# Kernel optimization log

Hardware: AMD Instinct MI355X
Metric: run time of the kernel (lower is better)

## Reference

```python
import jax, jax.numpy as jnp
import numpy as np

NUM_ITEMS, NUM_USERS, H = 100000, 16384, 48
GCN, ATTN, HID, TOW = 128, 128, 256, 256


def setup_inputs() -> dict:
    key = jax.random.key(0)
    ks = jax.random.split(key, 20)
    s = 0.02
    return {
        'item_feat': jax.random.normal(ks[0], (NUM_ITEMS, 2), jnp.float32),
        'gcn_item_emb': jax.random.normal(ks[1], (NUM_ITEMS, GCN), jnp.float32),
        'gcn_user_emb': jax.random.normal(ks[2], (NUM_USERS, GCN), jnp.float32),
        'hist_idx': jax.random.randint(ks[3], (NUM_USERS, H), 0, NUM_ITEMS, jnp.int32),
        'hist_len': jax.random.randint(ks[4], (NUM_USERS,), 0, H, jnp.int32),
        'Wi1': s * jax.random.normal(ks[5], (GCN + 2, HID), jnp.float32),
        'bi1': jnp.zeros((HID,), jnp.float32),
        'Wi2': s * jax.random.normal(ks[6], (HID, TOW), jnp.float32),
        'bi2': jnp.zeros((TOW,), jnp.float32),
        'Wq': s * jax.random.normal(ks[7], (GCN, ATTN), jnp.float32),
        'bq': jnp.zeros((ATTN,), jnp.float32),
        'Wk': s * jax.random.normal(ks[8], (TOW, ATTN), jnp.float32),
        'bk': jnp.zeros((ATTN,), jnp.float32),
        'Wu1': s * jax.random.normal(ks[9], (GCN + TOW, HID), jnp.float32),
        'bu1': jnp.zeros((HID,), jnp.float32),
        'Wu2': s * jax.random.normal(ks[10], (HID, TOW), jnp.float32),
        'bu2': jnp.zeros((TOW,), jnp.float32),
    }


def _l2norm(x):
    # F.normalize(dim=1): divide by L2 norm clamped to 1e-12
    n = jnp.sqrt(jnp.sum(x * x, axis=1, keepdims=True))
    return x / jnp.maximum(n, 1e-12)


def reference(item_feat, gcn_item_emb, gcn_user_emb, hist_idx, hist_len,
              Wi1, bi1, Wi2, bi2, Wq, bq, Wk, bk, Wu1, bu1, Wu2, bu2):
    # encode_items: [N, 130] -> MLP -> normalized [N, TOW]
    xi = jnp.concatenate([item_feat, gcn_item_emb], axis=1)
    h = jax.nn.relu(xi @ Wi1 + bi1)
    item_emb = _l2norm(h @ Wi2 + bi2)

    # encode_users (batched ragged attention with padding mask)
    item_vecs = item_emb[hist_idx]                       # [U, H, TOW]
    q = gcn_user_emb @ Wq + bq                           # [U, ATTN]
    k = item_vecs @ Wk + bk                              # [U, H, ATTN]
    scores = jnp.einsum('ud,uhd->uh', q, k) / jnp.sqrt(jnp.float32(ATTN))
    mask = jnp.arange(H)[None, :] <= hist_len[:, None]   # >= 1 valid per user
    attn = jax.nn.softmax(jnp.where(mask, scores, -1e30), axis=1)
    hist = jnp.einsum('uh,uhd->ud', attn, item_vecs)     # [U, TOW]
    fused = jnp.concatenate([gcn_user_emb, hist], axis=1)  # [U, 384]
    hu = jax.nn.relu(fused @ Wu1 + bu1)
    user_emb = _l2norm(hu @ Wu2 + bu2)
    return user_emb
```

## Files before the change

### kernel.cpp

```cpp
#include <hip/hip_runtime.h>
#include <hip/hip_bf16.h>
#include <hip/hip_fp8.h>
#include <math.h>

#define NITEMS 100000
#define NUSERS 16384
#define HLEN   48
#define GCN    128
#define ATTN_D 128
#define HID    256
#define TOW    256

typedef __attribute__((ext_vector_type(8))) short short8;
typedef __attribute__((ext_vector_type(16))) unsigned char uchar16;
typedef __attribute__((ext_vector_type(4))) float f32x4;
typedef __hip_bfloat16 bf16;

static __device__ __forceinline__ float bfu(unsigned short u) {
  unsigned int x = ((unsigned int)u) << 16;
  float f; __builtin_memcpy(&f, &x, 4); return f;
}
static __device__ __forceinline__ short f2bf(float v) {
  bf16 h = __float2bfloat16(v);
  short s; __builtin_memcpy(&s, &h, 2); return s;
}
static __device__ __forceinline__ unsigned char f2e4m3(float v) {
  __hip_fp8_e4m3 t(v);
  return (unsigned char)t.__x;
}
static __device__ __forceinline__ float e4m3f(unsigned char b) {
  __hip_fp8_e4m3 t;
  t.__x = (__hip_fp8_storage_t)b;
  return (float)t;
}

#define GLDS16(g, l)                                                            \
  __builtin_amdgcn_global_load_lds(                                             \
      (const __attribute__((address_space(1))) unsigned int*)(g),               \
      (__attribute__((address_space(3))) unsigned int*)(l), 16, 0, 0)

__global__ __launch_bounds__(256) void k_prep_w(const float* __restrict__ W,
                                                bf16* __restrict__ out,
                                                int Korig, int KS, int NT, int perm) {
  int tid = blockIdx.x * 256 + threadIdx.x;
  int total = KS * NT * 512;
  if (tid >= total) return;
  int i  = tid & 7;
  int l  = (tid >> 3) & 63;
  int ct = (tid >> 9) % NT;
  int ks = (tid >> 9) / NT;
  int k   = ks * 32 + ((l >> 4) << 3) + i;
  int col = ct * 16 + (l & 15);
  int N = NT * 16;
  int srck = perm ? ((k < 128) ? (k + 2) : (k - 128)) : k;
  float v = (k < Korig) ? W[(size_t)srck * N + col] : 0.f;
  out[tid] = __float2bfloat16(v);
}

__global__ __launch_bounds__(256) void k_prep_w8(const float* __restrict__ W,
                                                 unsigned char* __restrict__ out,
                                                 int KS, int NT) {
  int tid = blockIdx.x * 256 + threadIdx.x;
  int total = KS * NT * 512;
  if (tid >= total) return;
  int i  = tid & 7;
  int l  = (tid >> 3) & 63;
  int ct = (tid >> 9) % NT;
  int ks = (tid >> 9) / NT;
  int k   = ks * 32 + ((l >> 4) << 3) + i;
  int col = ct * 16 + (l & 15);
  out[tid] = f2e4m3(W[(size_t)k * (NT * 16) + col]);
}

__global__ __launch_bounds__(256) void k_prep_user(const float* __restrict__ gcn_user,
                                                   bf16* __restrict__ fused) {
  int tid = blockIdx.x * 256 + threadIdx.x;
  if (tid >= NUSERS * GCN) return;
  int k = tid & 127;
  int u = tid >> 7;
  fused[(size_t)u * (GCN + TOW) + k] = __float2bfloat16(gcn_user[tid]);
}

__global__ __launch_bounds__(256) void k_fold(const float* __restrict__ Wq,
                                              const float* __restrict__ Wk,
                                              const float* __restrict__ bq,
                                              float* __restrict__ out) {
  const float INV_S = 0.08838834764831845f;
  const int t = threadIdx.x;
  const int b = blockIdx.x;
  if (b < 16) {
    __shared__ float wq[8][128];
    for (int s = t; s < 8 * 128; s += 256)
      wq[s >> 7][s & 127] = Wq[(size_t)(b * 8 + (s >> 7)) * ATTN_D + (s & 127)];
    __syncthreads();
    float acc[8] = {0.f, 0.f, 0.f, 0.f, 0.f, 0.f, 0.f, 0.f};
    for (int d = 0; d < 128; ++d) {
      const float wk = Wk[(size_t)t * ATTN_D + d];
      #pragma unroll
      for (int gg = 0; gg < 8; ++gg) acc[gg] = fmaf(wq[gg][d], wk, acc[gg]);
    }
    #pragma unroll
    for (int gg = 0; gg < 8; ++gg)
      out[(size_t)(b * 8 + gg) * TOW + t] = acc[gg] * INV_S;
  } else {
    float a = 0.f;
    for (int d = 0; d < 128; ++d)
      a = fmaf(bq[d], Wk[(size_t)t * ATTN_D + d], a);
    out[(size_t)128 * TOW + t] = a * INV_S;
  }
}

__global__ __launch_bounds__(512, 4) void k_item_g1(
    const float* __restrict__ feat,
    const float* __restrict__ gcn,
    const bf16* __restrict__ Wf,
    const float* __restrict__ Wi1raw,
    const float* __restrict__ bias,
    unsigned char* __restrict__ h_out,
    int ntiles)
{
  __shared__ bf16  bs[4 * 8192];
  __shared__ float wfeat[512];
  const int j = threadIdx.x;
  const int l = j & 63;
  const int w = j >> 6;
  const int r = l & 15, g = l >> 4;
  const int jb = (j & ~63) * 8;

  #pragma unroll
  for (int s = 0; s < 8; ++s)
    GLDS16(Wf + (size_t)s * 4096 + (size_t)j * 8, &bs[s * 4096 + jb]);
  wfeat[j] = Wi1raw[j];

  float bj[16];
  #pragma unroll
  for (int ct = 0; ct < 16; ++ct) bj[ct] = bias[ct * 16 + r];

  __syncthreads();

  for (int t = blockIdx.x; t < ntiles; t += gridDim.x) {
    const int R0 = t * 128 + w * 16;
    int arow = R0 + r; if (arow >= NITEMS) arow = NITEMS - 1;
    const float* grow = gcn + (size_t)arow * GCN;

    f32x4 acc[16];
    #pragma unroll
    for (int ct = 0; ct < 16; ++ct) acc[ct] = (f32x4){0.f, 0.f, 0.f, 0.f};

    #pragma unroll 1
    for (int ks = 0; ks < 4; ++ks) {
      const float4* p = (const float4*)(grow + ks * 32 + g * 8);
      float4 x = p[0], y = p[1];
      short8 a;
      a[0] = f2bf(x.x); a[1] = f2bf(x.y); a[2] = f2bf(x.z); a[3] = f2bf(x.w);
      a[4] = f2bf(y.x); a[5] = f2bf(y.y); a[6] = f2bf(y.z); a[7] = f2bf(y.w);
      const bf16* wb = bs + (size_t)(ks * 16) * 512 + (size_t)l * 8;
      #pragma unroll
      for (int ct = 0; ct < 16; ++ct) {
        short8 b = *(const short8*)(wb + ct * 512);
        acc[ct] = __builtin_amdgcn_mfma_f32_16x16x32_bf16(a, b, acc[ct], 0, 0, 0);
      }
    }

    float f0[4], f1[4];
    #pragma unroll
    for (int i = 0; i < 4; ++i) {
      int orow = R0 + g * 4 + i; if (orow >= NITEMS) orow = NITEMS - 1;
      float2 fv = *(const float2*)(feat + (size_t)orow * 2);
      f0[i] = fv.x; f1[i] = fv.y;
    }
    #pragma unroll
    for (int ct = 0; ct < 16; ++ct) {
      const float w0 = wfeat[ct * 16 + r];
      const float w1 = wfeat[256 + ct * 16 + r];
      #pragma unroll
      for (int i = 0; i < 4; ++i) {
        float v = acc[ct][i] + bj[ct];
        v = fmaf(f0[i], w0, v);
        v = fmaf(f1[i], w1, v);
        h_out[(size_t)(R0 + g * 4 + i) * 256 + ct * 16 + r] =
            f2e4m3(fmaxf(v, 0.f));
      }
    }
  }
}

__global__ __launch_bounds__(512, 4) void k_gemm2_f8(
    const unsigned char* __restrict__ A8,
    const unsigned char* __restrict__ Wf8,
    const float* __restrict__ bias,
    unsigned char* __restrict__ Cout,
    int ntiles)
{
  __shared__ unsigned char bs8[8 * 8192];
  const int j = threadIdx.x;
  const int l = j & 63;
  const int w = j >> 6;
  const int r = l & 15, g = l >> 4;
  const int jb = (j & ~63) * 16;

  #pragma unroll
  for (int s = 0; s < 8; ++s)
    GLDS16(Wf8 + (size_t)s * 8192 + (size_t)j * 16, &bs8[s * 8192 + jb]);

  __syncthreads();

  for (int t = blockIdx.x; t < ntiles; t += gridDim.x) {
    const int R0 = t * 128 + w * 16;
    const unsigned char* arow = A8 + (size_t)(R0 + r) * 256 + g * 8;
    const unsigned char* wbase = bs8 + (size_t)l * 8;

    f32x4 acc[16];
    #pragma unroll
    for (int ct = 0; ct < 16; ++ct) acc[ct] = (f32x4){0.f, 0.f, 0.f, 0.f};

    #pragma unroll 1
    for (int ks = 0; ks < 8; ++ks) {
      long a;
      __builtin_memcpy(&a, arow + ks * 32, 8);
      const unsigned char* wb = wbase + (size_t)(ks * 16) * 512;
      #pragma unroll
      for (int ct = 0; ct < 16; ++ct) {
        long b;
        __builtin_memcpy(&b, wb + ct * 512, 8);
        acc[ct] = __builtin_amdgcn_mfma_f32_16x16x32_fp8_fp8(a, b, acc[ct], 0, 0, 0);
      }
    }

    float s[4] = {0.f, 0.f, 0.f, 0.f};
    #pragma unroll
    for (int ct = 0; ct < 16; ++ct) {
      const float bj = bias[ct * 16 + r];
      #pragma unroll
      for (int i = 0; i < 4; ++i) {
        acc[ct][i] += bj;
        s[i] += acc[ct][i] * acc[ct][i];
      }
    }
    #pragma unroll
    for (int off = 1; off < 16; off <<= 1) {
      #pragma unroll
      for (int i = 0; i < 4; ++i) s[i] += __shfl_xor(s[i], off);
    }
    float rn[4];
    #pragma unroll
    for (int i = 0; i < 4; ++i) rn[i] = 1.f / fmaxf(sqrtf(s[i]), 1e-12f);
    #pragma unroll
    for (int ct = 0; ct < 16; ++ct)
      #pragma unroll
      for (int i = 0; i < 4; ++i)
        Cout[(size_t)(R0 + g * 4 + i) * 256 + ct * 16 + r] =
            f2e4m3(acc[ct][i] * rn[i]);
  }
}

template<int KS, int NT, int MODE, int MR>
__global__ __launch_bounds__(256) void k_gemm(
    const bf16* __restrict__ A,
    const bf16* __restrict__ Wf,
    const float* __restrict__ bias,
    void* __restrict__ Cout,
    int Mtiles, int Astride)
{
  static_assert(NT % 4 == 0, "NT must be divisible by 4");
  constexpr int BSZ = NT * 512;
  constexpr int CH  = NT / 4;
  __shared__ bf16 bs[2][BSZ];
  const int j   = threadIdx.x;
  const int l   = j & 63;
  const int wid = j >> 6;
  int tile = blockIdx.x * 4 + wid;
  if (tile >= Mtiles) tile = Mtiles - 1;
  const int N = NT * 16;
  const int r = l & 15, g = l >> 4;

  {
    const short8* src = (const short8*)Wf;
    short8* dst = (short8*)bs[0];
    #pragma unroll
    for (int c = 0; c < CH; ++c) dst[c * 256 + j] = src[c * 256 + j];
  }

  f32x4 acc[MR][NT];
  #pragma unroll
  for (int mr = 0; mr < MR; ++mr)
    #pragma unroll
    for (int ct = 0; ct < NT; ++ct) acc[mr][ct] = (f32x4){0.f, 0.f, 0.f, 0.f};

  const bf16* arow[MR];
  #pragma unroll
  for (int mr = 0; mr < MR; ++mr)
    arow[mr] = A + (size_t)(tile * (16 * MR) + mr * 16 + r) * Astride + g * 8;

  __syncthreads();

  #pragma unroll
  for (int ks = 0; ks < KS; ++ks) {
    const int cur = ks & 1;
    short8 a[MR];
    #pragma unroll
    for (int mr = 0; mr < MR; ++mr) a[mr] = *(const short8*)(arow[mr] + ks * 32);
    short8 st[CH];
    if (ks + 1 < KS) {
      const short8* src = (const short8*)(Wf + (size_t)(ks + 1) * BSZ);
      #pragma unroll
      for (int c = 0; c < CH; ++c) st[c] = src[c * 256 + j];
    }
    const bf16* wb = bs[cur] + (size_t)l * 8;
    #pragma unroll
    for (int ct = 0; ct < NT; ++ct) {
      short8 b = *(const short8*)(wb + ct * 512);
      #pragma unroll
      for (int mr = 0; mr < MR; ++mr)
        acc[mr][ct] = __builtin_amdgcn_mfma_f32_16x16x32_bf16(a[mr], b, acc[mr][ct], 0, 0, 0);
    }
    if (ks + 1 < KS) {
      short8* dst = (short8*)bs[cur ^ 1];
      #pragma unroll
      for (int c = 0; c < CH; ++c) dst[c * 256 + j] = st[c];
    }
    __syncthreads();
  }

  #pragma unroll
  for (int mr = 0; mr < MR; ++mr) {
    #pragma unroll
    for (int ct = 0; ct < NT; ++ct) {
      const float bj = bias[ct * 16 + r];
      #pragma unroll
      for (int i = 0; i < 4; ++i) acc[mr][ct][i] += bj;
    }
  }

  if (MODE == 0 || MODE == 2 || MODE == 4) {
    #pragma unroll
    for (int mr = 0; mr < MR; ++mr)
      #pragma unroll
      for (int ct = 0; ct < NT; ++ct)
        #pragma unroll
        for (int i = 0; i < 4; ++i) {
          float v = acc[mr][ct][i];
          if (MODE == 0) v = fmaxf(v, 0.f);
          size_t off = (size_t)(tile * (16 * MR) + mr * 16 + g * 4 + i) * N + ct * 16 + r;
          if (MODE == 4) ((float*)Cout)[off] = v;
          else           ((bf16*)Cout)[off]  = __float2bfloat16(v);
        }
  } else {
    #pragma unroll
    for (int mr = 0; mr < MR; ++mr) {
      float s[4] = {0.f, 0.f, 0.f, 0.f};
      #pragma unroll
      for (int ct = 0; ct < NT; ++ct)
        #pragma unroll
        for (int i = 0; i < 4; ++i) s[i] += acc[mr][ct][i] * acc[mr][ct][i];
      #pragma unroll
      for (int off = 1; off < 16; off <<= 1) {
        #pragma unroll
        for (int i = 0; i < 4; ++i) s[i] += __shfl_xor(s[i], off);
      }
      float rn[4];
      #pragma unroll
      for (int i = 0; i < 4; ++i) rn[i] = 1.f / fmaxf(sqrtf(s[i]), 1e-12f);
      #pragma unroll
      for (int ct = 0; ct < NT; ++ct)
        #pragma unroll
        for (int i = 0; i < 4; ++i) {
          size_t off = (size_t)(tile * (16 * MR) + mr * 16 + g * 4 + i) * N + ct * 16 + r;
          float v = acc[mr][ct][i] * rn[i];
          if (MODE == 3) ((float*)Cout)[off] = v;
          else           ((bf16*)Cout)[off]  = __float2bfloat16(v);
        }
    }
  }
}

__global__ __launch_bounds__(256) void k_user_attn(
    const float* __restrict__ Qt,
    const int*   __restrict__ hist_idx,
    const int*   __restrict__ hist_len,
    const unsigned char* __restrict__ emb8,
    bf16* __restrict__ fused)
{
  const int u = blockIdx.x;
  const int j = threadIdx.x;
  const int wid = j >> 6, lane = j & 63;
  const int g = lane >> 4, r = lane & 15;
  const int part = wid * 4 + g;
  __shared__ int   idx[HLEN];
  __shared__ float redO[16][TOW + 4];
  __shared__ float redL[16];

  const int nv = hist_len[u] + 1;

  if (j < HLEN) idx[j] = hist_idx[u * HLEN + j];
  const float* qp = Qt + (size_t)u * TOW + r * 16;
  f32x4 q0 = *(const f32x4*)(qp);
  f32x4 q1 = *(const f32x4*)(qp + 4);
  f32x4 q2 = *(const f32x4*)(qp + 8);
  f32x4 q3 = *(const f32x4*)(qp + 12);
  __syncthreads();

  float l = 0.f;
  f32x4 O0 = (f32x4){0.f,0.f,0.f,0.f}, O1 = O0, O2 = O0, O3 = O0;

  for (int h = part; h < nv; h += 16) {
    const uchar16 e = *(const uchar16*)(emb8 + (size_t)idx[h] * TOW + r * 16);
    float ef[16];
    #pragma unroll
    for (int i = 0; i < 16; ++i) ef[i] = e4m3f(e[i]);

    float sc = q0.x*ef[0] + q0.y*ef[1] + q0.z*ef[2] + q0.w*ef[3]
             + q1.x*ef[4] + q1.y*ef[5] + q1.z*ef[6] + q1.w*ef[7]
             + q2.x*ef[8] + q2.y*ef[9] + q2.z*ef[10]+ q2.w*ef[11]
             + q3.x*ef[12]+ q3.y*ef[13]+ q3.z*ef[14]+ q3.w*ef[15];
    #pragma unroll
    for (int off = 1; off < 16; off <<= 1) sc += __shfl_xor(sc, off);
    const float p = __expf(sc);
    l += p;
    O0.x += p*ef[0];  O0.y += p*ef[1];  O0.z += p*ef[2];  O0.w += p*ef[3];
    O1.x += p*ef[4];  O1.y += p*ef[5];  O1.z += p*ef[6];  O1.w += p*ef[7];
    O2.x += p*ef[8];  O2.y += p*ef[9];  O2.z += p*ef[10]; O2.w += p*ef[11];
    O3.x += p*ef[12]; O3.y += p*ef[13]; O3.z += p*ef[14]; O3.w += p*ef[15];
  }

  *(f32x4*)(&redO[part][r * 16])      = O0;
  *(f32x4*)(&redO[part][r * 16 + 4])  = O1;
  *(f32x4*)(&redO[part][r * 16 + 8])  = O2;
  *(f32x4*)(&redO[part][r * 16 + 12]) = O3;
  if (r == 0) redL[part] = l;
  __syncthreads();

  float L = 0.f, val = 0.f;
  #pragma unroll
  for (int w = 0; w < 16; ++w) {
    L   += redL[w];
    val += redO[w][j];
  }
  fused[(size_t)u * (GCN + TOW) + GCN + j] = __float2bfloat16(val / L);
}

extern "C" void kernel_launch(void* const* d_in, const int* in_sizes, int n_in,
                              void* d_out, int out_size, void* d_ws, size_t ws_size,
                              hipStream_t stream) {
  const float* item_feat = (const float*)d_in[0];
  const float* gcn_item  = (const float*)d_in[1];
  const float* gcn_user  = (const float*)d_in[2];
  const int*   hist_idx  = (const int*)d_in[3];
  const int*   hist_len  = (const int*)d_in[4];
  const float* Wi1 = (const float*)d_in[5];
  const float* bi1 = (const float*)d_in[6];
  const float* Wi2 = (const float*)d_in[7];
  const float* bi2 = (const float*)d_in[8];
  const float* Wq  = (const float*)d_in[9];
  const float* bq  = (const float*)d_in[10];
  const float* Wk  = (const float*)d_in[11];
  const float* bk  = (const float*)d_in[12];
  const float* Wu1 = (const float*)d_in[13];
  const float* bu1 = (const float*)d_in[14];
  const float* Wu2 = (const float*)d_in[15];
  const float* bu2 = (const float*)d_in[16];
  (void)bk;

  char* ws = (char*)d_ws;
  bf16*  Wi1p  = (bf16*)(ws + 0);
  unsigned char* Wi2p8 = (unsigned char*)(ws + 81920);
  bf16*  Wu1p  = (bf16*)(ws + 147456);
  bf16*  Wu2p  = (bf16*)(ws + 344064);
  float* Wqkf  = (float*)(ws + 475136);
  bf16*  Wqkp  = (bf16*)(ws + 607232);
  float* Qt    = (float*)(ws + 672768);
  unsigned char* h8   = (unsigned char*)(ws + 17449984);
  unsigned char* emb8 = (unsigned char*)(ws + 43074560);
  bf16*  fusedA   = (bf16*)(ws + 68699136);
  bf16*  hu_buf   = (bf16*)(ws + 81282048);

  k_prep_w<<<160, 256, 0, stream>>>(Wi1, Wi1p, 130, 5, 16, 1);
  k_prep_w8<<<256, 256, 0, stream>>>(Wi2, Wi2p8, 8, 16);
  k_prep_w<<<384, 256, 0, stream>>>(Wu1, Wu1p, 384, 12, 16, 0);
  k_prep_w<<<256, 256, 0, stream>>>(Wu2, Wu2p, 256, 8, 16, 0);
  k_fold<<<17, 256, 0, stream>>>(Wq, Wk, bq, Wqkf);
  k_prep_w<<<128, 256, 0, stream>>>(Wqkf, Wqkp, 128, 4, 16, 0);
  k_prep_user<<<8192, 256, 0, stream>>>(gcn_user, fusedA);

  const int i128 = (NITEMS + 127) / 128;
  k_item_g1<<<512, 512, 0, stream>>>(item_feat, gcn_item, Wi1p, Wi1, bi1, h8, i128);
  k_gemm2_f8<<<512, 512, 0, stream>>>(h8, Wi2p8, bi2, emb8, i128);

  const int utiles = NUSERS / 32;
  const int ublk = utiles / 4;
  k_gemm<4, 16, 4, 2><<<ublk, 256, 0, stream>>>(fusedA, Wqkp, Wqkf + 128 * 256, Qt, utiles, 384);
  k_user_attn<<<NUSERS, 256, 0, stream>>>(Qt, hist_idx, hist_len, emb8, fusedA);
  k_gemm<12, 16, 0, 2><<<ublk, 256, 0, stream>>>(fusedA, Wu1p, bu1, hu_buf, utiles, 384);
  k_gemm<8, 16, 3, 2><<<ublk, 256, 0, stream>>>(hu_buf, Wu2p, bu2, (float*)d_out, utiles, 256);
}
```

Measured before the change: 148.7 us.

## Map one wavefront per user in attention kernel with shuffle reduction and prefetch

The user attention kernel now gives each 64-lane wavefront one user, with four users per block, instead of spreading one user over a whole 256-thread block. The cross-partition reduction moves from shared memory plus two block barriers to wavefront xor-shuffles. Each lane also prefetches its next fp8 history row while computing the current one, and writes bf16 output as 16-byte vectors. Each wave now walks up to 12 history steps serially rather than 3, so there is less parallelism within a user in exchange for removing the barriers, the LDS traffic and most idle threads on short histories.

```diff
diff --git a/kernel.cpp b/kernel.cpp
--- a/kernel.cpp
+++ b/kernel.cpp
@@ -381,30 +381,29 @@
     const unsigned char* __restrict__ emb8,
     bf16* __restrict__ fused)
 {
-  const int u = blockIdx.x;
-  const int j = threadIdx.x;
-  const int wid = j >> 6, lane = j & 63;
+  const int wid = threadIdx.x >> 6, lane = threadIdx.x & 63;
+  const int u = blockIdx.x * 4 + wid;
   const int g = lane >> 4, r = lane & 15;
-  const int part = wid * 4 + g;
-  __shared__ int   idx[HLEN];
-  __shared__ float redO[16][TOW + 4];
-  __shared__ float redL[16];
-
   const int nv = hist_len[u] + 1;
-
-  if (j < HLEN) idx[j] = hist_idx[u * HLEN + j];
+  const int* uidx = hist_idx + (size_t)u * HLEN;
+
   const float* qp = Qt + (size_t)u * TOW + r * 16;
   f32x4 q0 = *(const f32x4*)(qp);
   f32x4 q1 = *(const f32x4*)(qp + 4);
   f32x4 q2 = *(const f32x4*)(qp + 8);
   f32x4 q3 = *(const f32x4*)(qp + 12);
-  __syncthreads();
 
   float l = 0.f;
   f32x4 O0 = (f32x4){0.f,0.f,0.f,0.f}, O1 = O0, O2 = O0, O3 = O0;
 
-  for (int h = part; h < nv; h += 16) {
-    const uchar16 e = *(const uchar16*)(emb8 + (size_t)idx[h] * TOW + r * 16);
+  int h = g;
+  uchar16 e = (uchar16){0,0,0,0,0,0,0,0,0,0,0,0,0,0,0,0};
+  if (h < nv)
+    e = *(const uchar16*)(emb8 + (size_t)uidx[h] * TOW + r * 16);
+  for (; h < nv; h += 4) {
+    uchar16 en = (uchar16){0,0,0,0,0,0,0,0,0,0,0,0,0,0,0,0};
+    if (h + 4 < nv)
+      en = *(const uchar16*)(emb8 + (size_t)uidx[h + 4] * TOW + r * 16);
     float ef[16];
     #pragma unroll
     for (int i = 0; i < 16; ++i) ef[i] = e4m3f(e[i]);
@@ -421,22 +420,35 @@
     O1.x += p*ef[4];  O1.y += p*ef[5];  O1.z += p*ef[6];  O1.w += p*ef[7];
     O2.x += p*ef[8];  O2.y += p*ef[9];  O2.z += p*ef[10]; O2.w += p*ef[11];
     O3.x += p*ef[12]; O3.y += p*ef[13]; O3.z += p*ef[14]; O3.w += p*ef[15];
-  }
-
-  *(f32x4*)(&redO[part][r * 16])      = O0;
-  *(f32x4*)(&redO[part][r * 16 + 4])  = O1;
-  *(f32x4*)(&redO[part][r * 16 + 8])  = O2;
-  *(f32x4*)(&redO[part][r * 16 + 12]) = O3;
-  if (r == 0) redL[part] = l;
-  __syncthreads();
-
-  float L = 0.f, val = 0.f;
-  #pragma unroll
-  for (int w = 0; w < 16; ++w) {
-    L   += redL[w];
-    val += redO[w][j];
-  }
-  fused[(size_t)u * (GCN + TOW) + GCN + j] = __float2bfloat16(val / L);
+    e = en;
+  }
+
+  #pragma unroll
+  for (int off = 16; off < 64; off <<= 1) {
+    l += __shfl_xor(l, off);
+    #pragma unroll
+    for (int i = 0; i < 4; ++i) {
+      O0[i] += __shfl_xor(O0[i], off);
+      O1[i] += __shfl_xor(O1[i], off);
+      O2[i] += __shfl_xor(O2[i], off);
+      O3[i] += __shfl_xor(O3[i], off);
+    }
+  }
+
+  if (g == 0) {
+    const float inv = 1.f / l;
+    short8 o0, o1;
+    #pragma unroll
+    for (int i = 0; i < 4; ++i) {
+      o0[i]     = f2bf(O0[i] * inv);
+      o0[4 + i] = f2bf(O1[i] * inv);
+      o1[i]     = f2bf(O2[i] * inv);
+      o1[4 + i] = f2bf(O3[i] * inv);
+    }
+    bf16* dst = fused + (size_t)u * (GCN + TOW) + GCN + r * 16;
+    *(short8*)dst       = o0;
+    *(short8*)(dst + 8) = o1;
+  }
 }
 
 extern "C" void kernel_launch(void* const* d_in, const int* in_sizes, int n_in,
@@ -489,7 +501,7 @@
   const int utiles = NUSERS / 32;
   const int ublk = utiles / 4;
   k_gemm<4, 16, 4, 2><<<ublk, 256, 0, stream>>>(fusedA, Wqkp, Wqkf + 128 * 256, Qt, utiles, 384);
-  k_user_attn<<<NUSERS, 256, 0, stream>>>(Qt, hist_idx, hist_len, emb8, fusedA);
+  k_user_attn<<<NUSERS / 4, 256, 0, stream>>>(Qt, hist_idx, hist_len, emb8, fusedA);
   k_gemm<12, 16, 0, 2><<<ublk, 256, 0, stream>>>(fusedA, Wu1p, bu1, hu_buf, utiles, 384);
   k_gemm<8, 16, 3, 2><<<ublk, 256, 0, stream>>>(hu_buf, Wu2p, bu2, (float*)d_out, utiles, 256);
 }
```

After: 142.0 us. 4.5% less time.
